# Optimization experiments

Measured on AMD Instinct MI355X. Metric: run time of the kernel, lower is better.

Reference implementation:

```python
import jax, jax.numpy as jnp
import numpy as np

D_MODEL = 512
N_HEADS = 8
ATTN_UNITS = 64
FF_UNITS = 2048
LN_EPS = 1e-3  # keras LayerNormalization default epsilon


def setup_inputs() -> dict:
    key = jax.random.key(0)
    ks = jax.random.split(key, 12)

    def glorot(k, shape):
        fan_in, fan_out = shape[-2], shape[-1]
        std = jnp.sqrt(2.0 / (fan_in + fan_out)).astype(jnp.float32)
        return jax.random.normal(k, shape, dtype=jnp.float32) * std

    x = jax.random.normal(ks[0], (8, 1024, D_MODEL), dtype=jnp.float32)
    qw = glorot(ks[1], (N_HEADS, D_MODEL, ATTN_UNITS))
    kw = glorot(ks[2], (N_HEADS, D_MODEL, ATTN_UNITS))
    vw = glorot(ks[3], (N_HEADS, D_MODEL, D_MODEL))
    lw = glorot(ks[4], (N_HEADS * D_MODEL, D_MODEL))
    w1 = glorot(ks[5], (D_MODEL, FF_UNITS))
    b1 = jax.random.normal(ks[6], (FF_UNITS,), dtype=jnp.float32) * 0.02
    w2 = glorot(ks[7], (FF_UNITS, D_MODEL))
    b2 = jax.random.normal(ks[8], (D_MODEL,), dtype=jnp.float32) * 0.02
    gamma1 = jnp.ones((D_MODEL,), dtype=jnp.float32)
    beta1 = jnp.zeros((D_MODEL,), dtype=jnp.float32)
    gamma2 = jnp.ones((D_MODEL,), dtype=jnp.float32)
    beta2 = jnp.zeros((D_MODEL,), dtype=jnp.float32)
    return {"x": x, "qw": qw, "kw": kw, "vw": vw, "lw": lw,
            "gamma1": gamma1, "beta1": beta1,
            "w1": w1, "b1": b1, "w2": w2, "b2": b2,
            "gamma2": gamma2, "beta2": beta2}


def _layer_norm(x, gamma, beta):
    mean = jnp.mean(x, axis=-1, keepdims=True)
    var = jnp.var(x, axis=-1, keepdims=True)
    return gamma * (x - mean) / jnp.sqrt(var + LN_EPS) + beta


def reference(x, qw, kw, vw, lw, gamma1, beta1, w1, b1, w2, b2, gamma2, beta2):
    B, S, D = x.shape
    H = qw.shape[0]
    scale = 1.0 / np.sqrt(D).astype(np.float32)

    # Batched per-head projections (replaces the Python loop over heads)
    q = jnp.einsum('bsd,hdu->bhsu', x, qw)      # [B,H,S,U]
    k = jnp.einsum('bsd,hdu->bhsu', x, kw)      # [B,H,S,U]
    v = jnp.einsum('bsd,hde->bhse', x, vw)      # [B,H,S,D]  (per-head value dim = D)

    scores = jnp.einsum('bhsu,bhtu->bhst', q, k) * scale  # [B,H,S,S]
    probs = jax.nn.softmax(scores, axis=-1)
    attn = jnp.einsum('bhst,bhte->bhse', probs, v)        # [B,H,S,D]

    # concat heads along feature axis, then output projection
    attn = attn.transpose(0, 2, 1, 3).reshape(B, S, H * D)
    mha = attn @ lw                                        # [B,S,D]

    # dropout in inference mode -> identity
    h = _layer_norm(x + mha, gamma1, beta1)

    ff = jax.nn.relu(h @ w1 + b1) @ w2 + b2
    out = _layer_norm(h + ff, gamma2, beta2)
    return out
```

## Files before the change

kernel.cpp:

```cpp
#include <hip/hip_runtime.h>
#include <stdint.h>


#define BM 128
#define BN 128
#define BK 64

typedef unsigned short u16;
typedef __attribute__((ext_vector_type(8))) short short8;
typedef __attribute__((ext_vector_type(4))) float f32x4;

__device__ __forceinline__ float bf2f(u16 b) {
  union { unsigned int u; float f; } c; c.u = ((unsigned int)b) << 16; return c.f;
}
__device__ __forceinline__ u16 f2bf(float f) {
  union { float f; unsigned int u; } c; c.f = f;
  unsigned int u = c.u;
  return (u16)((u + 0x7FFFu + ((u >> 16) & 1u)) >> 16);
}

#if __has_builtin(__builtin_amdgcn_exp2f)
#define EXP2(x) __builtin_amdgcn_exp2f(x)
#else
#define EXP2(x) exp2f(x)
#endif

#define GPTR(p) ((const __attribute__((address_space(1))) void*)(p))
#define LPTR(p) ((__attribute__((address_space(3))) void*)(p))

template<int EPI>
__launch_bounds__(256)
__global__ void gemm_bt(const u16* __restrict__ A, const u16* __restrict__ Bt,
                        void* __restrict__ Cv, const float* __restrict__ bias,
                        int K, int lda, int ldb, int ldc,
                        int batchInner,
                        long aOut, long aIn, long bOut, long bIn,
                        long cOut, long cIn, float scale, int swz)
{
  int bx = blockIdx.x, by = blockIdx.y, bz = blockIdx.z;
  if (swz == 1) {
    const int L = blockIdx.x + gridDim.x * blockIdx.y;
    const int xcd = L & 7;
    const int t = L >> 3;
    bx = t % gridDim.x;
    by = ((t / gridDim.x) << 3) | xcd;
  } else if (swz == 2) {
    const int L = blockIdx.x + gridDim.x * (blockIdx.y + gridDim.y * blockIdx.z);
    const int xcd = L & 7;
    const int t = L >> 3;
    const int G = gridDim.z >> 3;
    const int s = t % G;
    const int r = t / G;
    bz = (s << 3) | xcd;
    bx = r % gridDim.x;
    by = r / gridDim.x;
  }

  const int zo = bz / batchInner;
  const int zi = bz - zo * batchInner;
  A  += zo * aOut + zi * aIn;
  Bt += zo * bOut + zi * bIn;
  const long cOff = zo * cOut + zi * cIn;

  const int m0 = by * BM;
  const int n0 = bx * BN;

  __shared__ u16 As[BM * BK];
  __shared__ u16 Bs[BN * BK];

  const int tid  = threadIdx.x;
  const int wave = tid >> 6;
  const int lane = tid & 63;
  const int wr = (wave >> 1) << 6;
  const int wc = (wave & 1) << 6;

  const int rsub = lane >> 3;
  const int kch  = (((lane & 7) ^ rsub) << 3);
  const int cb   = wave << 2;

  const u16* gA[4]; const u16* gB[4]; u16* lA[4]; u16* lB[4];
  #pragma unroll
  for (int j = 0; j < 4; ++j) {
    const int c = cb + j;
    gA[j] = A  + (long)(m0 + (c << 3) + rsub) * lda + kch;
    gB[j] = Bt + (long)(n0 + (c << 3) + rsub) * ldb + kch;
    lA[j] = As + c * 512;
    lB[j] = Bs + c * 512;
  }

  const int fr = lane & 15;
  const int kq = lane >> 4;
  const u16* pA[4][2]; const u16* pB[4][2];
  #pragma unroll
  for (int i = 0; i < 4; ++i)
    #pragma unroll
    for (int ks = 0; ks < 2; ++ks) {
      const int slot = (((ks << 2) | kq) ^ (fr & 7)) << 3;
      pA[i][ks] = As + (wr + (i << 4) + fr) * BK + slot;
      pB[i][ks] = Bs + (wc + (i << 4) + fr) * BK + slot;
    }

  f32x4 acc[4][4];
  #pragma unroll
  for (int i = 0; i < 4; ++i)
    #pragma unroll
    for (int j = 0; j < 4; ++j)
      acc[i][j] = (f32x4){0.f, 0.f, 0.f, 0.f};

  const int kIter = K >> 6;
  for (int kt = 0; kt < kIter; ++kt) {
    __syncthreads();
    #pragma unroll
    for (int j = 0; j < 4; ++j) {
      __builtin_amdgcn_global_load_lds(GPTR(gA[j]), LPTR(lA[j]), 16, 0, 0);
      __builtin_amdgcn_global_load_lds(GPTR(gB[j]), LPTR(lB[j]), 16, 0, 0);
    }
    #pragma unroll
    for (int j = 0; j < 4; ++j) { gA[j] += BK; gB[j] += BK; }
    __syncthreads();

    #pragma unroll
    for (int ks = 0; ks < 2; ++ks) {
      short8 af[4], bfv[4];
      #pragma unroll
      for (int i = 0; i < 4; ++i) af[i]  = *(const short8*)pA[i][ks];
      #pragma unroll
      for (int i = 0; i < 4; ++i) bfv[i] = *(const short8*)pB[i][ks];
      #pragma unroll
      for (int mi = 0; mi < 4; ++mi)
        #pragma unroll
        for (int ni = 0; ni < 4; ++ni)
          acc[mi][ni] = __builtin_amdgcn_mfma_f32_16x16x32_bf16(
              af[mi], bfv[ni], acc[mi][ni], 0, 0, 0);
    }
  }

  const int rq = (lane >> 4) << 2;
  #pragma unroll
  for (int mi = 0; mi < 4; ++mi) {
    #pragma unroll
    for (int ni = 0; ni < 4; ++ni) {
      const int col = n0 + wc + (ni << 4) + fr;
      float bv = 0.f;
      if (EPI == 3 || EPI == 4) bv = bias[col];
      #pragma unroll
      for (int r = 0; r < 4; ++r) {
        const int row = m0 + wr + (mi << 4) + rq + r;
        float v = acc[mi][ni][r];
        if (EPI == 1) v *= scale;
        v += bv;
        if (EPI == 3) v = fmaxf(v, 0.f);
        if (EPI == 0 || EPI == 1 || EPI == 3)
          ((u16*)Cv + cOff)[(long)row * ldc + col] = f2bf(v);
        else
          ((float*)Cv + cOff)[(long)row * ldc + col] = v;
      }
    }
  }
}

__launch_bounds__(256, 2)
__global__ void attn_fused(const u16* __restrict__ QKb, const u16* __restrict__ Vtb,
                           u16* __restrict__ attn)
{
  const int L = blockIdx.x + (blockIdx.y << 1) + (blockIdx.z << 4);
  const int xcd = L & 7;
  const int t0 = L >> 3;
  const int bh = ((t0 & 7) << 3) | xcd;
  const int r0_ = t0 >> 3;
  const int b = bh >> 3, h = bh & 7;
  const int q0 = (r0_ >> 1) << 7;
  const int e0 = (r0_ & 1) << 8;

  __shared__ u16 QP[8192];
  __shared__ u16 Kl[4096];
  __shared__ u16 Vl[16384];
  __shared__ __align__(16) float stats[4][32];

  const int tid  = threadIdx.x;
  const int wave = tid >> 6;
  const int lane = tid & 63;
  const int rsub = lane >> 3;
  const int kch  = ((lane & 7) ^ rsub) << 3;
  const int fr = lane & 15;
  const int kq = lane >> 4;
  const int rq = kq << 2;

  const u16* Qg = QKb + ((long)(b << 10) + q0) * 1024 + (h << 6);
  #pragma unroll
  for (int j = 0; j < 4; ++j) {
    const int c = (wave << 2) + j;
    __builtin_amdgcn_global_load_lds(
        GPTR(Qg + (long)((c << 3) + rsub) * 1024 + kch),
        LPTR(QP + c * 512), 16, 0, 0);
  }
  __syncthreads();

  short8 qb[2][2];
  #pragma unroll
  for (int ni = 0; ni < 2; ++ni)
    #pragma unroll
    for (int ks = 0; ks < 2; ++ks) {
      const int row = (wave << 5) + (ni << 4) + fr;
      const int phys = (((ks << 2) | kq) ^ (fr & 7)) << 3;
      qb[ni][ks] = *(const short8*)(QP + row * 64 + phys);
    }

  u16* Pl = QP + (wave << 11);
  float* myStats = stats[wave];

  const u16* gK[2]; const u16* gV[8];
  #pragma unroll
  for (int j = 0; j < 2; ++j)
    gK[j] = QKb + ((long)(b << 10) + ((wave * 2 + j) << 3) + rsub) * 1024
                + 512 + (h << 6) + kch;
  #pragma unroll
  for (int j = 0; j < 8; ++j)
    gV[j] = Vtb + ((long)bh * 512 + e0 + ((wave * 8 + j) << 3) + rsub) * 1024 + kch;

  f32x4 o[2][16];
  #pragma unroll
  for (int mi = 0; mi < 2; ++mi)
    #pragma unroll
    for (int ni = 0; ni < 16; ++ni)
      o[mi][ni] = (f32x4){0.f, 0.f, 0.f, 0.f};
  float l_[2] = {0.f, 0.f};

  for (int tt = 0; tt < 16; ++tt) {
    __syncthreads();
    #pragma unroll
    for (int j = 0; j < 2; ++j)
      __builtin_amdgcn_global_load_lds(GPTR(gK[j]), LPTR(Kl + (wave * 2 + j) * 512), 16, 0, 0);
    #pragma unroll
    for (int j = 0; j < 8; ++j)
      __builtin_amdgcn_global_load_lds(GPTR(gV[j]), LPTR(Vl + (wave * 8 + j) * 512), 16, 0, 0);
    #pragma unroll
    for (int j = 0; j < 2; ++j) gK[j] += 64 * 1024;
    #pragma unroll
    for (int j = 0; j < 8; ++j) gV[j] += 64;
    __syncthreads();

    f32x4 st[4][2];
    #pragma unroll
    for (int mi = 0; mi < 4; ++mi)
      #pragma unroll
      for (int ni = 0; ni < 2; ++ni)
        st[mi][ni] = (f32x4){0.f, 0.f, 0.f, 0.f};
    #pragma unroll
    for (int ks = 0; ks < 2; ++ks) {
      const int phys = (((ks << 2) | kq) ^ (fr & 7)) << 3;
      short8 kf[4];
      #pragma unroll
      for (int mi = 0; mi < 4; ++mi)
        kf[mi] = *(const short8*)(Kl + ((mi << 4) + fr) * 64 + phys);
      #pragma unroll
      for (int mi = 0; mi < 4; ++mi)
        #pragma unroll
        for (int ni = 0; ni < 2; ++ni)
          st[mi][ni] = __builtin_amdgcn_mfma_f32_16x16x32_bf16(
              kf[mi], qb[ni][ks], st[mi][ni], 0, 0, 0);
    }

    #pragma unroll
    for (int ni = 0; ni < 2; ++ni) {
      const int qlocal = (ni << 4) + fr;
      u16* prow = Pl + qlocal * 64 + ((kq & 1) << 2);
      float rs = 0.f;
      #pragma unroll
      for (int mi = 0; mi < 4; ++mi) {
        const float p0 = EXP2(st[mi][ni][0]);
        const float p1 = EXP2(st[mi][ni][1]);
        const float p2 = EXP2(st[mi][ni][2]);
        const float p3 = EXP2(st[mi][ni][3]);
        rs += (p0 + p1) + (p2 + p3);
        const int chunk = ((((mi << 1) | (kq >> 1)) ^ (qlocal & 7)) << 3);
        uint2 pk;
        pk.x = (uint32_t)f2bf(p0) | ((uint32_t)f2bf(p1) << 16);
        pk.y = (uint32_t)f2bf(p2) | ((uint32_t)f2bf(p3) << 16);
        *(uint2*)(prow + chunk) = pk;
      }
      l_[ni] += rs;
    }

    #pragma unroll
    for (int ks = 0; ks < 2; ++ks) {
      const int phys = (((ks << 2) | kq) ^ (fr & 7)) << 3;
      short8 pa[2];
      pa[0] = *(const short8*)(Pl + fr * 64 + phys);
      pa[1] = *(const short8*)(Pl + (16 + fr) * 64 + phys);
      #pragma unroll
      for (int ni = 0; ni < 16; ++ni) {
        const short8 vb = *(const short8*)(Vl + ((ni << 4) + fr) * 64 + phys);
        o[0][ni] = __builtin_amdgcn_mfma_f32_16x16x32_bf16(pa[0], vb, o[0][ni], 0, 0, 0);
        o[1][ni] = __builtin_amdgcn_mfma_f32_16x16x32_bf16(pa[1], vb, o[1][ni], 0, 0, 0);
      }
    }
  }

  #pragma unroll
  for (int ni = 0; ni < 2; ++ni) {
    float s = l_[ni];
    s += __shfl_xor(s, 16);
    s += __shfl_xor(s, 32);
    l_[ni] = s;
  }
  if (kq == 0) {
    myStats[fr]      = 1.f / l_[0];
    myStats[16 + fr] = 1.f / l_[1];
  }
  f32x4 il[2];
  il[0] = *(const f32x4*)(myStats + rq);
  il[1] = *(const f32x4*)(myStats + 16 + rq);

  #pragma unroll
  for (int mi = 0; mi < 2; ++mi)
    #pragma unroll
    for (int ni = 0; ni < 16; ++ni) {
      const int col = (h << 9) + e0 + (ni << 4) + fr;
      #pragma unroll
      for (int r = 0; r < 4; ++r) {
        const long row = (long)(b << 10) + q0 + (wave << 5) + (mi << 4) + rq + r;
        attn[row * 4096 + col] = f2bf(o[mi][ni][r] * il[mi][r]);
      }
    }
}

__global__ void transpose_cast(const float* __restrict__ src, u16* __restrict__ dst,
                               int R, int C, long sBatch, long dBatch, float mul)
{
  __shared__ float tile[32][33];
  src += (long)blockIdx.z * sBatch;
  dst += (long)blockIdx.z * dBatch;
  const int c0 = blockIdx.x << 5, r0 = blockIdx.y << 5;
  const int tx = threadIdx.x, ty = threadIdx.y;
  #pragma unroll
  for (int i = 0; i < 32; i += 8) {
    int r = r0 + ty + i, c = c0 + tx;
    if (r < R && c < C) tile[ty + i][tx] = src[(long)r * C + c];
  }
  __syncthreads();
  #pragma unroll
  for (int i = 0; i < 32; i += 8) {
    int c = c0 + ty + i, r = r0 + tx;
    if (c < C && r < R) dst[(long)c * R + r] = f2bf(tile[tx][ty + i] * mul);
  }
}

__global__ void cast_bf16(const float* __restrict__ src, u16* __restrict__ dst, int n4)
{
  int t = blockIdx.x * blockDim.x + threadIdx.x;
  if (t < n4) {
    float4 v = ((const float4*)src)[t];
    uint2 o;
    o.x = (unsigned)f2bf(v.x) | ((unsigned)f2bf(v.y) << 16);
    o.y = (unsigned)f2bf(v.z) | ((unsigned)f2bf(v.w) << 16);
    ((uint2*)dst)[t] = o;
  }
}

__global__ void add_ln_red(const float* __restrict__ a, const float* __restrict__ P,
                           long pstride, int nsplit, const float* __restrict__ bias,
                           const float* __restrict__ gamma, const float* __restrict__ beta,
                           float* __restrict__ outF, u16* __restrict__ outB)
{
  const long row = blockIdx.x;
  const int tid = threadIdx.x;
  const int wave = tid >> 6, lane = tid & 63;
  float4 va = ((const float4*)(a + (row << 9)))[tid];
  float x0 = va.x, x1 = va.y, x2 = va.z, x3 = va.w;
  for (int sp = 0; sp < nsplit; ++sp) {
    float4 p = ((const float4*)(P + sp * pstride + (row << 9)))[tid];
    x0 += p.x; x1 += p.y; x2 += p.z; x3 += p.w;
  }
  if (bias) {
    float4 bv = ((const float4*)bias)[tid];
    x0 += bv.x; x1 += bv.y; x2 += bv.z; x3 += bv.w;
  }
  float s = x0 + x1 + x2 + x3;
  float q = x0*x0 + x1*x1 + x2*x2 + x3*x3;
  #pragma unroll
  for (int off = 32; off > 0; off >>= 1) {
    s += __shfl_xor(s, off);
    q += __shfl_xor(q, off);
  }
  __shared__ float red[4];
  if (lane == 0) { red[wave] = s; red[2 + wave] = q; }
  __syncthreads();
  s = red[0] + red[1]; q = red[2] + red[3];
  float mu  = s * (1.f / 512.f);
  float var = q * (1.f / 512.f) - mu * mu;
  float rstd = rsqrtf(var + 1e-3f);
  float4 g  = ((const float4*)gamma)[tid];
  float4 be = ((const float4*)beta)[tid];
  float o0 = g.x * (x0 - mu) * rstd + be.x;
  float o1 = g.y * (x1 - mu) * rstd + be.y;
  float o2 = g.z * (x2 - mu) * rstd + be.z;
  float o3 = g.w * (x3 - mu) * rstd + be.w;
  ((float4*)(outF + (row << 9)))[tid] = make_float4(o0, o1, o2, o3);
  if (outB) {
    uint2 o;
    o.x = (unsigned)f2bf(o0) | ((unsigned)f2bf(o1) << 16);
    o.y = (unsigned)f2bf(o2) | ((unsigned)f2bf(o3) << 16);
    ((uint2*)(outB + (row << 9)))[tid] = o;
  }
}

extern "C" void kernel_launch(void* const* d_in, const int* in_sizes, int n_in,
                              void* d_out, int out_size, void* d_ws, size_t ws_size,
                              hipStream_t stream)
{
  (void)in_sizes; (void)n_in; (void)out_size;
  const float* x      = (const float*)d_in[0];
  const float* qw     = (const float*)d_in[1];
  const float* kw     = (const float*)d_in[2];
  const float* vw     = (const float*)d_in[3];
  const float* lw     = (const float*)d_in[4];
  const float* gamma1 = (const float*)d_in[5];
  const float* beta1  = (const float*)d_in[6];
  const float* w1     = (const float*)d_in[7];
  const float* b1     = (const float*)d_in[8];
  const float* w2     = (const float*)d_in[9];
  const float* b2     = (const float*)d_in[10];
  const float* gamma2 = (const float*)d_in[11];
  const float* beta2  = (const float*)d_in[12];

  const int Bb = 8, S = 1024, D = 512, H = 8, F = 2048;
  const int N = Bb * S;
  const float qmul = 0.04419417382415922f * 1.4426950408889634f;

  char* w = (char*)d_ws;
  size_t off = 0;
  auto alloc = [&](size_t bytes) -> char* {
    char* p = w + off; off += (bytes + 255) & ~(size_t)255; return p;
  };
  u16* Xbf  = (u16*)alloc((size_t)N * D * 2);
  u16* WqkT = (u16*)alloc((size_t)2 * D * D * 2);
  u16* WvT  = (u16*)alloc((size_t)H * D * D * 2);
  u16* lwT  = (u16*)alloc((size_t)D * (H * D) * 2);
  u16* w1T  = (u16*)alloc((size_t)F * D * 2);
  u16* w2T  = (u16*)alloc((size_t)D * F * 2);
  char* qkArena = alloc((size_t)N * 2 * D * 2);
  char* bigArena = alloc((size_t)N * (H * D) * 2);
  const size_t fixedEnd = off;

  u16*   QKb  = (u16*)qkArena;
  u16*   attn = (u16*)bigArena;
  float* hbuf = (float*)bigArena;
  u16*   hbf  = (u16*)(bigArena + (size_t)N * D * 4);
  u16*   ff1  = (u16*)(bigArena + (size_t)N * D * 4 + (size_t)N * D * 2);

  u16*   Vtb = (u16*)(w + fixedEnd);
  const long pstride = (long)N * D;
  int SK = (ws_size - fixedEnd >= (size_t)4 * pstride * 4) ? 4 : 1;
  float* part = (float*)(w + fixedEnd);

  dim3 tb(32, 8);
  cast_bf16<<<dim3(N * D / 4 / 256), 256, 0, stream>>>(x, Xbf, N * D / 4);
  transpose_cast<<<dim3(2, 16, 8),  tb, 0, stream>>>(qw, WqkT, 512, 64, 32768, 32768, qmul);
  transpose_cast<<<dim3(2, 16, 8),  tb, 0, stream>>>(kw, WqkT + (size_t)D * D, 512, 64, 32768, 32768, 1.f);
  transpose_cast<<<dim3(16, 16, 8), tb, 0, stream>>>(vw, WvT, 512, 512, 262144, 262144, 1.f);
  transpose_cast<<<dim3(16, 128, 1),tb, 0, stream>>>(lw, lwT, 4096, 512, 0, 0, 1.f);
  transpose_cast<<<dim3(64, 16, 1), tb, 0, stream>>>(w1, w1T, 512, 2048, 0, 0, 1.f);
  transpose_cast<<<dim3(16, 64, 1), tb, 0, stream>>>(w2, w2T, 2048, 512, 0, 0, 1.f);

  gemm_bt<0><<<dim3(8, 64, 1), 256, 0, stream>>>(Xbf, WqkT, QKb, nullptr,
      512, 512, 512, 1024, 1, 0, 0, 0, 0, 0, 0, 0.f, 1);

  gemm_bt<0><<<dim3(8, 4, 64), 256, 0, stream>>>(WvT, Xbf, Vtb, nullptr,
      512, 512, 512, 1024, H,
      0, (long)D * D,
      (long)S * D, 0,
      (long)H * D * S, (long)D * S, 0.f, 2);

  attn_fused<<<dim3(2, 8, 64), 256, 0, stream>>>(QKb, Vtb, attn);

  gemm_bt<2><<<dim3(4, 64, SK), 256, 0, stream>>>(attn, lwT, part, nullptr,
      4096 / SK, 4096, 4096, 512, 1,
      4096 / SK, 0, 4096 / SK, 0, pstride, 0, 0.f, 1);

  add_ln_red<<<dim3(N), 128, 0, stream>>>(x, part, pstride, SK, nullptr,
                                          gamma1, beta1, hbuf, hbf);

  gemm_bt<3><<<dim3(16, 64, 1), 256, 0, stream>>>(hbf, w1T, ff1, b1,
      512, 512, 512, 2048, 1, 0, 0, 0, 0, 0, 0, 0.f, 1);

  gemm_bt<2><<<dim3(4, 64, SK), 256, 0, stream>>>(ff1, w2T, part, nullptr,
      2048 / SK, 2048, 2048, 512, 1,
      2048 / SK, 0, 2048 / SK, 0, pstride, 0, 0.f, 1);

  add_ln_red<<<dim3(N), 128, 0, stream>>>(hbuf, part, pstride, SK, b2,
                                          gamma2, beta2, (float*)d_out, nullptr);
}
```

Before: 443.4 us.

## Repartition attention PV product across waves by value columns with shared P tile

The PV stage is restructured so each wave owns a 64-column slice of the value dimension across all 128 query rows, instead of 32 query rows across all 256 columns. Every wave writes its P slice into one shared LDS tile and reads all of it after an added barrier, so each wave reads only its own V columns rather than the full V tile. The aim is less LDS read traffic per wave, at the cost of an extra block-wide sync per key tile and a block-wide sync before the normalized store. The XCD-aware batch swizzle for the V projection GEMM is also removed and replaced with default ordering.

```diff
diff --git a/kernel.cpp b/kernel.cpp
--- a/kernel.cpp
+++ b/kernel.cpp
@@ -37,23 +37,14 @@
                         long aOut, long aIn, long bOut, long bIn,
                         long cOut, long cIn, float scale, int swz)
 {
-  int bx = blockIdx.x, by = blockIdx.y, bz = blockIdx.z;
+  int bx = blockIdx.x, by = blockIdx.y;
+  const int bz = blockIdx.z;
   if (swz == 1) {
     const int L = blockIdx.x + gridDim.x * blockIdx.y;
     const int xcd = L & 7;
     const int t = L >> 3;
     bx = t % gridDim.x;
     by = ((t / gridDim.x) << 3) | xcd;
-  } else if (swz == 2) {
-    const int L = blockIdx.x + gridDim.x * (blockIdx.y + gridDim.y * blockIdx.z);
-    const int xcd = L & 7;
-    const int t = L >> 3;
-    const int G = gridDim.z >> 3;
-    const int s = t % G;
-    const int r = t / G;
-    bz = (s << 3) | xcd;
-    bx = r % gridDim.x;
-    by = r / gridDim.x;
   }
 
   const int zo = bz / batchInner;
@@ -175,7 +166,7 @@
   __shared__ u16 QP[8192];
   __shared__ u16 Kl[4096];
   __shared__ u16 Vl[16384];
-  __shared__ __align__(16) float stats[4][32];
+  __shared__ __align__(16) float stats[128];
 
   const int tid  = threadIdx.x;
   const int wave = tid >> 6;
@@ -206,8 +197,7 @@
       qb[ni][ks] = *(const short8*)(QP + row * 64 + phys);
     }
 
-  u16* Pl = QP + (wave << 11);
-  float* myStats = stats[wave];
+  u16* Pl = QP;
 
   const u16* gK[2]; const u16* gV[8];
   #pragma unroll
@@ -218,12 +208,12 @@
   for (int j = 0; j < 8; ++j)
     gV[j] = Vtb + ((long)bh * 512 + e0 + ((wave * 8 + j) << 3) + rsub) * 1024 + kch;
 
-  f32x4 o[2][16];
-  #pragma unroll
-  for (int mi = 0; mi < 2; ++mi)
-    #pragma unroll
-    for (int ni = 0; ni < 16; ++ni)
-      o[mi][ni] = (f32x4){0.f, 0.f, 0.f, 0.f};
+  f32x4 o[8][4];
+  #pragma unroll
+  for (int qt = 0; qt < 8; ++qt)
+    #pragma unroll
+    for (int ni = 0; ni < 4; ++ni)
+      o[qt][ni] = (f32x4){0.f, 0.f, 0.f, 0.f};
   float l_[2] = {0.f, 0.f};
 
   for (int tt = 0; tt < 16; ++tt) {
@@ -264,7 +254,7 @@
     #pragma unroll
     for (int ni = 0; ni < 2; ++ni) {
       const int qlocal = (ni << 4) + fr;
-      u16* prow = Pl + qlocal * 64 + ((kq & 1) << 2);
+      u16* prow = Pl + ((wave << 5) + qlocal) * 64 + ((kq & 1) << 2);
       float rs = 0.f;
       #pragma unroll
       for (int mi = 0; mi < 4; ++mi) {
@@ -282,17 +272,22 @@
       l_[ni] += rs;
     }
 
+    __syncthreads();
+
     #pragma unroll
     for (int ks = 0; ks < 2; ++ks) {
       const int phys = (((ks << 2) | kq) ^ (fr & 7)) << 3;
-      short8 pa[2];
-      pa[0] = *(const short8*)(Pl + fr * 64 + phys);
-      pa[1] = *(const short8*)(Pl + (16 + fr) * 64 + phys);
-      #pragma unroll
-      for (int ni = 0; ni < 16; ++ni) {
-        const short8 vb = *(const short8*)(Vl + ((ni << 4) + fr) * 64 + phys);
-        o[0][ni] = __builtin_amdgcn_mfma_f32_16x16x32_bf16(pa[0], vb, o[0][ni], 0, 0, 0);
-        o[1][ni] = __builtin_amdgcn_mfma_f32_16x16x32_bf16(pa[1], vb, o[1][ni], 0, 0, 0);
+      short8 vb[4];
+      #pragma unroll
+      for (int ni = 0; ni < 4; ++ni)
+        vb[ni] = *(const short8*)(Vl + ((wave << 6) + (ni << 4) + fr) * 64 + phys);
+      #pragma unroll
+      for (int qt = 0; qt < 8; ++qt) {
+        const short8 pa = *(const short8*)(Pl + ((qt << 4) + fr) * 64 + phys);
+        #pragma unroll
+        for (int ni = 0; ni < 4; ++ni)
+          o[qt][ni] = __builtin_amdgcn_mfma_f32_16x16x32_bf16(
+              pa, vb[ni], o[qt][ni], 0, 0, 0);
       }
     }
   }
@@ -305,24 +300,24 @@
     l_[ni] = s;
   }
   if (kq == 0) {
-    myStats[fr]      = 1.f / l_[0];
-    myStats[16 + fr] = 1.f / l_[1];
-  }
-  f32x4 il[2];
-  il[0] = *(const f32x4*)(myStats + rq);
-  il[1] = *(const f32x4*)(myStats + 16 + rq);
-
-  #pragma unroll
-  for (int mi = 0; mi < 2; ++mi)
-    #pragma unroll
-    for (int ni = 0; ni < 16; ++ni) {
-      const int col = (h << 9) + e0 + (ni << 4) + fr;
+    stats[(wave << 5) + fr]      = 1.f / l_[0];
+    stats[(wave << 5) + 16 + fr] = 1.f / l_[1];
+  }
+  __syncthreads();
+
+  #pragma unroll
+  for (int qt = 0; qt < 8; ++qt) {
+    const f32x4 il = *(const f32x4*)(stats + (qt << 4) + rq);
+    #pragma unroll
+    for (int ni = 0; ni < 4; ++ni) {
+      const int col = (h << 9) + e0 + (wave << 6) + (ni << 4) + fr;
       #pragma unroll
       for (int r = 0; r < 4; ++r) {
-        const long row = (long)(b << 10) + q0 + (wave << 5) + (mi << 4) + rq + r;
-        attn[row * 4096 + col] = f2bf(o[mi][ni][r] * il[mi][r]);
+        const long row = (long)(b << 10) + q0 + (qt << 4) + rq + r;
+        attn[row * 4096 + col] = f2bf(o[qt][ni][r] * il[r]);
       }
     }
+  }
 }
 
 __global__ void transpose_cast(const float* __restrict__ src, u16* __restrict__ dst,
@@ -470,7 +465,7 @@
       512, 512, 512, 1024, H,
       0, (long)D * D,
       (long)S * D, 0,
-      (long)H * D * S, (long)D * S, 0.f, 2);
+      (long)H * D * S, (long)D * S, 0.f, 0);
 
   attn_fused<<<dim3(2, 8, 64), 256, 0, stream>>>(QKb, Vtb, attn);
 
```

After: 404.8 us. -8.7%, faster.
